# Performance work log

Hardware: AMD Instinct MI355X
Metric: run time of the kernel (lower is better)

Reference implementation:

```python
import jax, jax.numpy as jnp
import numpy as np

USER = 100000
ITEM = 50000
N = USER + ITEM
LATDIM = 64
IMG_DIM = 1024
E_ADJ = 3_000_000
E_IMG = 1_000_000
GNN_LAYERS = 2
RIS_LAMBDA = 1.0
EPS = 1e-12


def spmm(rows, cols, vals, x):
    # sparse [N,N] @ dense [N,D] via gather + segment-sum
    return jax.ops.segment_sum(vals[:, None] * x[cols], rows, num_segments=N)


def setup_inputs() -> dict:
    key = jax.random.key(0)
    ks = jax.random.split(key, 10)
    return {
        "adj_rows": jax.random.randint(ks[0], (E_ADJ,), 0, N, dtype=jnp.int32),
        "adj_cols": jax.random.randint(ks[1], (E_ADJ,), 0, N, dtype=jnp.int32),
        "adj_vals": jax.random.uniform(ks[2], (E_ADJ,), dtype=jnp.float32),
        "img_rows": jax.random.randint(ks[3], (E_IMG,), 0, N, dtype=jnp.int32),
        "img_cols": jax.random.randint(ks[4], (E_IMG,), 0, N, dtype=jnp.int32),
        "img_vals": jax.random.uniform(ks[5], (E_IMG,), dtype=jnp.float32),
        "image_embedding": jax.random.normal(ks[6], (ITEM, IMG_DIM), dtype=jnp.float32),
        "uEmbeds": jax.random.normal(ks[7], (USER, LATDIM), dtype=jnp.float32) * 0.01,
        "iEmbeds": jax.random.normal(ks[8], (ITEM, LATDIM), dtype=jnp.float32) * 0.01,
        "W_trans": jax.random.normal(ks[9], (IMG_DIM, LATDIM), dtype=jnp.float32) * (1.0 / np.sqrt(IMG_DIM)),
        "b_trans": jnp.zeros((LATDIM,), dtype=jnp.float32),
    }


def reference(adj_rows, adj_cols, adj_vals, img_rows, img_cols, img_vals,
              image_embedding, uEmbeds, iEmbeds, W_trans, b_trans):
    # trans == 1: Linear projection of image features
    image_feats = image_embedding @ W_trans + b_trans  # [ITEM, LATDIM]

    # image_adj @ concat(u, i)
    embeds_img_adj = spmm(img_rows, img_cols, img_vals, jnp.concatenate([uEmbeds, iEmbeds], axis=0))

    # F.normalize(image_feats) along dim=1 (L2, eps=1e-12)
    nrm = jnp.linalg.norm(image_feats, axis=1, keepdims=True)
    feats_n = image_feats / jnp.maximum(nrm, EPS)

    embeds_image = spmm(adj_rows, adj_cols, adj_vals, jnp.concatenate([uEmbeds, feats_n], axis=0))
    embeds_image_ = spmm(adj_rows, adj_cols, adj_vals,
                         jnp.concatenate([embeds_image[:USER], iEmbeds], axis=0))
    embeds_image = embeds_image + embeds_image_ + RIS_LAMBDA * embeds_img_adj

    # stacked GCN layers with sum over all layer outputs (including input)
    acc = embeds_image
    cur = embeds_image
    for _ in range(GNN_LAYERS):
        cur = spmm(adj_rows, adj_cols, adj_vals, cur)
        acc = acc + cur

    return acc[:USER], acc[USER:]
```

## Files before the change

### kernel.cpp

```cpp
#include <hip/hip_runtime.h>
#include <hip/hip_fp16.h>

#define USER_N 100000
#define ITEM_N 50000
#define NN (USER_N + ITEM_N)
#define D 64
#define IMGD 1024
#define LDP 68

#define BUCKET_BITS 10
#define BROWS (1 << BUCKET_BITS)
#define NBUCK ((NN + BROWS - 1) >> BUCKET_BITS)
#define CHUNK 4096

typedef _Float16 v4h __attribute__((ext_vector_type(4)));
typedef _Float16 v8h __attribute__((ext_vector_type(8)));
typedef float v4f __attribute__((ext_vector_type(4)));

__global__ __launch_bounds__(256) void wt_prep(
    const float* __restrict__ W, _Float16* __restrict__ Wt16)
{
    const int id = blockIdx.x * 256 + threadIdx.x;
    if (id >= D * IMGD) return;
    const int c = id >> 10;
    const int k = id & 1023;
    Wt16[id] = (_Float16)W[(size_t)k * D + c];
}

#define GAS 72
__global__ __launch_bounds__(256) void gemm_mfma(
    const float* __restrict__ A, const _Float16* __restrict__ Wt16,
    const float* __restrict__ b, float* __restrict__ C)
{
    __shared__ _Float16 Af[64][GAS];
    const int t = threadIdx.x;
    const int w = t >> 6;
    const int lane = t & 63;
    const int l16 = lane & 15;
    const int g = lane >> 4;
    const int row0 = blockIdx.x * 64;

    v4f acc[4] = {};

    const int lr = t >> 4;
    const int lk = (t & 15) * 4;

    for (int k0 = 0; k0 < IMGD; k0 += 64) {
#pragma unroll
        for (int i = 0; i < 4; i++) {
            const int r = lr + i * 16;
            const int grow = row0 + r;
            float4 v = make_float4(0.f, 0.f, 0.f, 0.f);
            if (grow < ITEM_N)
                v = *reinterpret_cast<const float4*>(&A[(size_t)grow * IMGD + k0 + lk]);
            v4h h;
            h[0] = (_Float16)v.x; h[1] = (_Float16)v.y;
            h[2] = (_Float16)v.z; h[3] = (_Float16)v.w;
            *reinterpret_cast<v4h*>(&Af[r][lk]) = h;
        }
        __syncthreads();
#pragma unroll
        for (int s = 0; s < 2; s++) {
            const int kb = s * 32;
            union { v8h v; v4h h[2]; } af;
            af.h[0] = *reinterpret_cast<const v4h*>(&Af[w * 16 + l16][kb + g * 4]);
            af.h[1] = *reinterpret_cast<const v4h*>(&Af[w * 16 + l16][kb + 16 + g * 4]);
#pragma unroll
            for (int n = 0; n < 4; n++) {
                const _Float16* wp = Wt16 + (size_t)(n * 16 + l16) * IMGD + k0 + kb + g * 4;
                union { v8h v; v4h h[2]; } bf;
                bf.h[0] = *reinterpret_cast<const v4h*>(wp);
                bf.h[1] = *reinterpret_cast<const v4h*>(wp + 16);
                acc[n] = __builtin_amdgcn_mfma_f32_16x16x32_f16(af.v, bf.v, acc[n], 0, 0, 0);
            }
        }
        __syncthreads();
    }
#pragma unroll
    for (int n = 0; n < 4; n++) {
        const int col = n * 16 + l16;
        const float bias = b[col];
#pragma unroll
        for (int r = 0; r < 4; r++) {
            const int grow = row0 + w * 16 + g * 4 + r;
            if (grow < ITEM_N)
                C[(size_t)grow * D + col] = acc[n][r] + bias;
        }
    }
}

__global__ __launch_bounds__(256) void gemm_feats32(
    const float* __restrict__ A, const float* __restrict__ W,
    const float* __restrict__ b, float* __restrict__ C)
{
    __shared__ float As[32][LDP];
    __shared__ float Ws[64][LDP];
    const int row0 = blockIdx.x * 32;
    const int t = threadIdx.x;
    const int tx = t & 15, ty = t >> 4;
    float acc[2][4] = {};

    const int lr = t >> 4;
    const int lk = (t & 15) * 4;

    for (int k0 = 0; k0 < IMGD; k0 += 64) {
#pragma unroll
        for (int i = 0; i < 2; i++) {
            const int r = lr + i * 16;
            const int grow = row0 + r;
            float4 v = make_float4(0.f, 0.f, 0.f, 0.f);
            if (grow < ITEM_N)
                v = *reinterpret_cast<const float4*>(&A[(size_t)grow * IMGD + k0 + lk]);
            *reinterpret_cast<float4*>(&As[r][lk]) = v;
        }
#pragma unroll
        for (int i = 0; i < 4; i++) {
            const int kr = lr + i * 16;
            float4 v = *reinterpret_cast<const float4*>(&W[(size_t)(k0 + kr) * D + lk]);
            *reinterpret_cast<float4*>(&Ws[kr][lk]) = v;
        }
        __syncthreads();
#pragma unroll
        for (int kb = 0; kb < 16; kb++) {
            float a_[2][4], w_[4][4];
#pragma unroll
            for (int i = 0; i < 2; i++) {
                const float4 v = *reinterpret_cast<const float4*>(&As[ty * 2 + i][kb * 4]);
                a_[i][0] = v.x; a_[i][1] = v.y; a_[i][2] = v.z; a_[i][3] = v.w;
            }
#pragma unroll
            for (int j = 0; j < 4; j++) {
                const float4 v = *reinterpret_cast<const float4*>(&Ws[kb * 4 + j][tx * 4]);
                w_[j][0] = v.x; w_[j][1] = v.y; w_[j][2] = v.z; w_[j][3] = v.w;
            }
#pragma unroll
            for (int j = 0; j < 4; j++)
#pragma unroll
                for (int i = 0; i < 2; i++)
#pragma unroll
                    for (int c = 0; c < 4; c++)
                        acc[i][c] += a_[i][j] * w_[j][c];
        }
        __syncthreads();
    }
    const float4 bias = *reinterpret_cast<const float4*>(&b[tx * 4]);
#pragma unroll
    for (int i = 0; i < 2; i++) {
        const int grow = row0 + ty * 2 + i;
        if (grow < ITEM_N) {
            float4 v;
            v.x = acc[i][0] + bias.x;
            v.y = acc[i][1] + bias.y;
            v.z = acc[i][2] + bias.z;
            v.w = acc[i][3] + bias.w;
            *reinterpret_cast<float4*>(&C[(size_t)grow * D + tx * 4]) = v;
        }
    }
}

__global__ __launch_bounds__(256) void rownorm_h(
    const float* __restrict__ X, __half* __restrict__ Y, int nrows)
{
    const int gid = blockIdx.x * blockDim.x + threadIdx.x;
    const int row = gid >> 6;
    const int lane = threadIdx.x & 63;
    if (row >= nrows) return;
    float v = X[(size_t)row * D + lane];
    float s = v * v;
#pragma unroll
    for (int o = 32; o > 0; o >>= 1) s += __shfl_xor(s, o, 64);
    const float scale = 1.0f / fmaxf(sqrtf(s), 1e-12f);
    Y[(size_t)row * D + lane] = __float2half(v * scale);
}

__global__ __launch_bounds__(256) void rownorm(float* __restrict__ X, int nrows)
{
    const int gid = blockIdx.x * blockDim.x + threadIdx.x;
    const int row = gid >> 6;
    const int lane = threadIdx.x & 63;
    if (row >= nrows) return;
    float v = X[(size_t)row * D + lane];
    float s = v * v;
#pragma unroll
    for (int o = 32; o > 0; o >>= 1) s += __shfl_xor(s, o, 64);
    const float scale = 1.0f / fmaxf(sqrtf(s), 1e-12f);
    X[(size_t)row * D + lane] = v * scale;
}

__global__ __launch_bounds__(256) void cvt_f2h(
    const float* __restrict__ s, __half* __restrict__ d, int n4)
{
    const int i = blockIdx.x * blockDim.x + threadIdx.x;
    if (i >= n4) return;
    const float4 v = reinterpret_cast<const float4*>(s)[i];
    __half2* d2 = reinterpret_cast<__half2*>(d);
    d2[2 * i]     = __floats2half2_rn(v.x, v.y);
    d2[2 * i + 1] = __floats2half2_rn(v.z, v.w);
}

__global__ __launch_bounds__(256) void bucket_count(
    const int* __restrict__ rows, int nnz, int nb, int* __restrict__ histT)
{
    __shared__ int cnt[NBUCK];
    for (int i = threadIdx.x; i < NBUCK; i += 256) cnt[i] = 0;
    __syncthreads();
    const int e0 = blockIdx.x * CHUNK;
    const int e1 = min(e0 + CHUNK, nnz);
    for (int e = e0 + threadIdx.x; e < e1; e += 256)
        atomicAdd(&cnt[rows[e] >> BUCKET_BITS], 1);
    __syncthreads();
    for (int b = threadIdx.x; b < NBUCK; b += 256)
        histT[b * nb + blockIdx.x] = cnt[b];
}

__global__ __launch_bounds__(1024) void scanA(
    const int* __restrict__ cnt, int* __restrict__ excl,
    int* __restrict__ blocksums, int n)
{
    const int t = threadIdx.x;
    const int gid = blockIdx.x * 1024 + t;
    const int lane = t & 63, wid = t >> 6;
    int v = (gid < n) ? cnt[gid] : 0;
    int x = v;
#pragma unroll
    for (int o = 1; o < 64; o <<= 1) {
        int y = __shfl_up(x, o, 64);
        if (lane >= o) x += y;
    }
    __shared__ int ws[16];
    __shared__ int wo[16];
    if (lane == 63) ws[wid] = x;
    __syncthreads();
    if (t < 16) {
        int s = ws[t];
        int xx = s;
#pragma unroll
        for (int o = 1; o < 16; o <<= 1) {
            int y = __shfl_up(xx, o, 16);
            if (t >= o) xx += y;
        }
        wo[t] = xx - s;
        if (t == 15) blocksums[blockIdx.x] = xx;
    }
    __syncthreads();
    if (gid < n) excl[gid] = x - v + wo[wid];
}

__global__ __launch_bounds__(1024) void scanB(int* __restrict__ bs, int nb)
{
    const int t = threadIdx.x;
    const int lane = t & 63, wid = t >> 6;
    int v = (t < nb) ? bs[t] : 0;
    int x = v;
#pragma unroll
    for (int o = 1; o < 64; o <<= 1) {
        int y = __shfl_up(x, o, 64);
        if (lane >= o) x += y;
    }
    __shared__ int ws[16];
    __shared__ int wo[16];
    if (lane == 63) ws[wid] = x;
    __syncthreads();
    if (t < 16) {
        int s = ws[t];
        int xx = s;
#pragma unroll
        for (int o = 1; o < 16; o <<= 1) {
            int y = __shfl_up(xx, o, 16);
            if (t >= o) xx += y;
        }
        wo[t] = xx - s;
    }
    __syncthreads();
    if (t < nb) bs[t] = x - v + wo[wid];
}

__global__ __launch_bounds__(256) void scan_apply(
    int* __restrict__ excl, const int* __restrict__ bo, int n)
{
    const int gid = blockIdx.x * blockDim.x + threadIdx.x;
    if (gid < n) excl[gid] += bo[gid >> 10];
}

__global__ __launch_bounds__(256) void bucket_place(
    const int* __restrict__ rows, const int* __restrict__ cols,
    const float* __restrict__ vals, int nnz, int nb,
    const int* __restrict__ offsT, uint2* __restrict__ rec)
{
    __shared__ int cur[NBUCK];
    for (int b = threadIdx.x; b < NBUCK; b += 256)
        cur[b] = offsT[b * nb + blockIdx.x];
    __syncthreads();
    const int e0 = blockIdx.x * CHUNK;
    const int e1 = min(e0 + CHUNK, nnz);
    for (int e = e0 + threadIdx.x; e < e1; e += 256) {
        const int r = rows[e];
        const int b = r >> BUCKET_BITS;
        const int pos = atomicAdd(&cur[b], 1);
        rec[pos] = make_uint2(((unsigned)cols[e] << BUCKET_BITS) |
                                  (unsigned)(r & (BROWS - 1)),
                              __float_as_uint(vals[e]));
    }
}

__global__ __launch_bounds__(1024) void bucket_finalize(
    const uint2* __restrict__ rec, int nnz, int nb,
    const int* __restrict__ offsT, int* __restrict__ rp,
    int2* __restrict__ ev)
{
    const int b = blockIdx.x;
    const int t = threadIdx.x;
    const int rlo = b << BUCKET_BITS;
    const int segs = offsT[b * nb];
    const int sege = (b + 1 < NBUCK) ? offsT[(b + 1) * nb] : nnz;

    __shared__ int cnt[BROWS];
    __shared__ int cur[BROWS];
    cnt[t] = 0;
    __syncthreads();
    for (int i = segs + t; i < sege; i += 1024)
        atomicAdd(&cnt[rec[i].x & (BROWS - 1)], 1);
    __syncthreads();

    const int lane = t & 63, wid = t >> 6;
    const int v = cnt[t];
    int x = v;
#pragma unroll
    for (int o = 1; o < 64; o <<= 1) {
        int y = __shfl_up(x, o, 64);
        if (lane >= o) x += y;
    }
    __shared__ int wsum[16];
    __shared__ int woff[16];
    if (lane == 63) wsum[wid] = x;
    __syncthreads();
    if (t < 16) {
        int s = wsum[t];
        int xx = s;
#pragma unroll
        for (int o = 1; o < 16; o <<= 1) {
            int y = __shfl_up(xx, o, 16);
            if (t >= o) xx += y;
        }
        woff[t] = xx - s;
    }
    __syncthreads();
    const int start = segs + (x - v + woff[wid]);

    if (rlo + t < NN) rp[rlo + t] = start;
    if (b == NBUCK - 1 && t == 0) rp[NN] = nnz;
    cur[t] = start;
    __syncthreads();

    for (int i = segs + t; i < sege; i += 1024) {
        const uint2 R = rec[i];
        const int rl = (int)(R.x & (BROWS - 1));
        const int c = (int)(R.x >> BUCKET_BITS);
        const int pos = atomicAdd(&cur[rl], 1);
        ev[pos] = make_int2(c, (int)R.y);
    }
}

__global__ __launch_bounds__(256) void spmm_h4(
    const int* __restrict__ rp, const int2* __restrict__ ev,
    const __half* __restrict__ src,
    float* __restrict__ out32, __half* __restrict__ out16, int limit16,
    const float* __restrict__ add1, const float* __restrict__ add2)
{
    const int wid = (blockIdx.x * 256 + threadIdx.x) >> 6;
    const int lane = threadIdx.x & 63;
    const int sub = lane >> 4;
    const int l16 = lane & 15;
    const int rowbase = wid * 4;
    if (rowbase >= NN) return;
    const int row = rowbase + sub;

    int v = 0;
    if (lane <= 4 && rowbase + lane <= NN) v = rp[rowbase + lane];
    const int s = __shfl(v, sub, 64);
    const int e = __shfl(v, sub + 1, 64);

    const __half* srcl = src + l16 * 4;
    float4 acc = make_float4(0.f, 0.f, 0.f, 0.f);

    union cvt { unsigned u; __half2 h; };
    int i = s;
    for (; i + 3 < e; i += 4) {
        const int2 E0 = ev[i], E1 = ev[i + 1], E2 = ev[i + 2], E3 = ev[i + 3];
        const uint2 g0 = *reinterpret_cast<const uint2*>(srcl + (size_t)E0.x * D);
        const uint2 g1 = *reinterpret_cast<const uint2*>(srcl + (size_t)E1.x * D);
        const uint2 g2 = *reinterpret_cast<const uint2*>(srcl + (size_t)E2.x * D);
        const uint2 g3 = *reinterpret_cast<const uint2*>(srcl + (size_t)E3.x * D);
#pragma unroll
        for (int k = 0; k < 4; k++) {
            const uint2 g = k == 0 ? g0 : k == 1 ? g1 : k == 2 ? g2 : g3;
            const float w = __int_as_float(k == 0 ? E0.y : k == 1 ? E1.y
                                           : k == 2 ? E2.y : E3.y);
            cvt c0, c1; c0.u = g.x; c1.u = g.y;
            const float2 f0 = __half22float2(c0.h);
            const float2 f1 = __half22float2(c1.h);
            acc.x += w * f0.x;
            acc.y += w * f0.y;
            acc.z += w * f1.x;
            acc.w += w * f1.y;
        }
    }
    for (; i < e; i++) {
        const int2 E0 = ev[i];
        const uint2 g = *reinterpret_cast<const uint2*>(srcl + (size_t)E0.x * D);
        const float w = __int_as_float(E0.y);
        cvt c0, c1; c0.u = g.x; c1.u = g.y;
        const float2 f0 = __half22float2(c0.h);
        const float2 f1 = __half22float2(c1.h);
        acc.x += w * f0.x;
        acc.y += w * f0.y;
        acc.z += w * f1.x;
        acc.w += w * f1.y;
    }

    if (row >= NN) return;
    const size_t idx = (size_t)row * D + l16 * 4;
    if (add1) {
        const float4 a = *reinterpret_cast<const float4*>(&add1[idx]);
        acc.x += a.x; acc.y += a.y; acc.z += a.z; acc.w += a.w;
    }
    if (add2) {
        const float4 a = *reinterpret_cast<const float4*>(&add2[idx]);
        acc.x += a.x; acc.y += a.y; acc.z += a.z; acc.w += a.w;
    }
    *reinterpret_cast<float4*>(&out32[idx]) = acc;
    if (row < limit16) {
        const __half2 o0 = __floats2half2_rn(acc.x, acc.y);
        const __half2 o1 = __floats2half2_rn(acc.z, acc.w);
        cvt c0, c1; c0.h = o0; c1.h = o1;
        *reinterpret_cast<uint2*>(&out16[idx]) = make_uint2(c0.u, c1.u);
    }
}

__global__ __launch_bounds__(256) void spmm_csr(
    const int* __restrict__ rp, const int2* __restrict__ ev,
    const float* __restrict__ srcU, const float* __restrict__ srcI,
    float* __restrict__ out,
    const float* __restrict__ add1, const float* __restrict__ add2)
{
    const int gid = blockIdx.x * blockDim.x + threadIdx.x;
    const int row = gid >> 6;
    const int lane = threadIdx.x & 63;
    if (row >= NN) return;
    const int s = rp[row], e = rp[row + 1];
    float acc = 0.f;
    int i = s;
    for (; i + 3 < e; i += 4) {
        const int2 e0 = ev[i], e1 = ev[i + 1], e2 = ev[i + 2], e3 = ev[i + 3];
        const float* p0 = (e0.x < USER_N) ? (srcU + (size_t)e0.x * D)
                                          : (srcI + (size_t)(e0.x - USER_N) * D);
        const float* p1 = (e1.x < USER_N) ? (srcU + (size_t)e1.x * D)
                                          : (srcI + (size_t)(e1.x - USER_N) * D);
        const float* p2 = (e2.x < USER_N) ? (srcU + (size_t)e2.x * D)
                                          : (srcI + (size_t)(e2.x - USER_N) * D);
        const float* p3 = (e3.x < USER_N) ? (srcU + (size_t)e3.x * D)
                                          : (srcI + (size_t)(e3.x - USER_N) * D);
        acc += __int_as_float(e0.y) * p0[lane];
        acc += __int_as_float(e1.y) * p1[lane];
        acc += __int_as_float(e2.y) * p2[lane];
        acc += __int_as_float(e3.y) * p3[lane];
    }
    for (; i < e; i++) {
        const int2 e0 = ev[i];
        const float* p0 = (e0.x < USER_N) ? (srcU + (size_t)e0.x * D)
                                          : (srcI + (size_t)(e0.x - USER_N) * D);
        acc += __int_as_float(e0.y) * p0[lane];
    }
    const size_t idx = (size_t)row * D + lane;
    if (add1) acc += add1[idx];
    if (add2) acc += add2[idx];
    out[idx] = acc;
}

extern "C" void kernel_launch(void* const* d_in, const int* in_sizes, int n_in,
                              void* d_out, int out_size, void* d_ws, size_t ws_size,
                              hipStream_t stream)
{
    const int*   adj_rows = (const int*)d_in[0];
    const int*   adj_cols = (const int*)d_in[1];
    const float* adj_vals = (const float*)d_in[2];
    const int*   img_rows = (const int*)d_in[3];
    const int*   img_cols = (const int*)d_in[4];
    const float* img_vals = (const float*)d_in[5];
    const float* img_emb  = (const float*)d_in[6];
    const float* uEmb     = (const float*)d_in[7];
    const float* iEmb     = (const float*)d_in[8];
    const float* Wt       = (const float*)d_in[9];
    const float* bt       = (const float*)d_in[10];
    float* out = (float*)d_out;

    const int e_adj = in_sizes[0];
    const int e_img = in_sizes[3];
    const int e_max = e_adj > e_img ? e_adj : e_img;
    const int NB_adj = (e_adj + CHUNK - 1) / CHUNK;
    const int NB_img = (e_img + CHUNK - 1) / CHUNK;
    const int NB_max = NB_adj > NB_img ? NB_adj : NB_img;

    const size_t ndbytes = (size_t)NN * D * sizeof(float);
    const size_t nhbytes = (size_t)NN * D * sizeof(__half);

    size_t off = 0;
    auto carve = [&](size_t bytes) { size_t p = off; off += (bytes + 255) & ~(size_t)255; return p; };
    char* base = (char*)d_ws;
    const size_t o_featsN = carve((size_t)ITEM_N * D * sizeof(float));
    const size_t o_bufA   = carve(ndbytes);
    const size_t o_bufB   = carve(ndbytes);
    const size_t o_rpAdj  = carve((NN + 1) * sizeof(int));
    const size_t o_rpImg  = carve((NN + 1) * sizeof(int));
    const size_t o_bsums  = carve(1024 * sizeof(int));
    const size_t o_histT  = carve((size_t)NBUCK * NB_max * sizeof(int));
    const size_t o_rec    = carve((size_t)e_max * sizeof(uint2) > nhbytes
                                      ? (size_t)e_max * sizeof(uint2) : nhbytes);
    const size_t o_evAdj  = carve((size_t)e_adj * sizeof(int2));
    const size_t need_base = off;
    const size_t o_evImg  = carve((size_t)e_img * sizeof(int2) > nhbytes
                                      ? (size_t)e_img * sizeof(int2) : nhbytes);
    const size_t o_x0     = carve(nhbytes);
    const size_t o_wt16   = carve((size_t)D * IMGD * sizeof(_Float16));
    const size_t need_h = off;

    if (ws_size < need_base) return;
    const bool use_h = (ws_size >= need_h);

    float* featsN = (float*)(base + o_featsN);
    float* bufA   = (float*)(base + o_bufA);
    float* bufB   = (float*)(base + o_bufB);
    int* rpAdj    = (int*)(base + o_rpAdj);
    int* rpImg    = (int*)(base + o_rpImg);
    int* bsums    = (int*)(base + o_bsums);
    int* histT    = (int*)(base + o_histT);
    uint2* rec    = (uint2*)(base + o_rec);
    int2* evAdj   = (int2*)(base + o_evAdj);
    int2* evImg   = (int2*)(base + o_evImg);
    __half* xC    = (__half*)(base + o_rec);
    __half* xB    = (__half*)(base + o_evImg);
    __half* x0    = (__half*)(base + o_x0);
    _Float16* wt16 = (_Float16*)(base + o_wt16);

    {
        const int n = NBUCK * NB_adj;
        const int nsb = (n + 1023) / 1024;
        bucket_count<<<NB_adj, 256, 0, stream>>>(adj_rows, e_adj, NB_adj, histT);
        scanA<<<nsb, 1024, 0, stream>>>(histT, histT, bsums, n);
        scanB<<<1, 1024, 0, stream>>>(bsums, nsb);
        scan_apply<<<(n + 255) / 256, 256, 0, stream>>>(histT, bsums, n);
        bucket_place<<<NB_adj, 256, 0, stream>>>(
            adj_rows, adj_cols, adj_vals, e_adj, NB_adj, histT, rec);
        bucket_finalize<<<NBUCK, 1024, 0, stream>>>(
            rec, e_adj, NB_adj, histT, rpAdj, evAdj);
    }
    {
        const int n = NBUCK * NB_img;
        const int nsb = (n + 1023) / 1024;
        bucket_count<<<NB_img, 256, 0, stream>>>(img_rows, e_img, NB_img, histT);
        scanA<<<nsb, 1024, 0, stream>>>(histT, histT, bsums, n);
        scanB<<<1, 1024, 0, stream>>>(bsums, nsb);
        scan_apply<<<(n + 255) / 256, 256, 0, stream>>>(histT, bsums, n);
        bucket_place<<<NB_img, 256, 0, stream>>>(
            img_rows, img_cols, img_vals, e_img, NB_img, histT, rec);
        bucket_finalize<<<NBUCK, 1024, 0, stream>>>(
            rec, e_img, NB_img, histT, rpImg, evImg);
    }

    const int SPMM4_GRID = (NN + 15) / 16;
    const int SPMM_GRID = (NN * 64 + 255) / 256;
    const int RN_GRID = (ITEM_N * 64 + 255) / 256;

    if (use_h) {
        __half* x0I = x0 + (size_t)USER_N * D;
        __half* xBI = xB + (size_t)USER_N * D;

        cvt_f2h<<<(USER_N * D / 4 + 255) / 256, 256, 0, stream>>>(
            uEmb, x0, USER_N * D / 4);
        cvt_f2h<<<(ITEM_N * D / 4 + 255) / 256, 256, 0, stream>>>(
            iEmb, x0I, ITEM_N * D / 4);

        spmm_h4<<<SPMM4_GRID, 256, 0, stream>>>(
            rpImg, evImg, x0, bufA, nullptr, 0, nullptr, nullptr);

        wt_prep<<<(D * IMGD + 255) / 256, 256, 0, stream>>>(Wt, wt16);
        gemm_mfma<<<(ITEM_N + 63) / 64, 256, 0, stream>>>(img_emb, wt16, bt, featsN);
        rownorm_h<<<RN_GRID, 256, 0, stream>>>(featsN, x0I, ITEM_N);

        cvt_f2h<<<(ITEM_N * D / 4 + 255) / 256, 256, 0, stream>>>(
            iEmb, xBI, ITEM_N * D / 4);

        spmm_h4<<<SPMM4_GRID, 256, 0, stream>>>(
            rpAdj, evAdj, x0, bufB, xB, USER_N, nullptr, nullptr);

        spmm_h4<<<SPMM4_GRID, 256, 0, stream>>>(
            rpAdj, evAdj, xB, bufA, xC, NN, bufB, bufA);

        spmm_h4<<<SPMM4_GRID, 256, 0, stream>>>(
            rpAdj, evAdj, xC, bufB, x0, NN, nullptr, nullptr);

        spmm_h4<<<SPMM4_GRID, 256, 0, stream>>>(
            rpAdj, evAdj, x0, out, nullptr, 0, bufA, bufB);
    } else {
        gemm_feats32<<<(ITEM_N + 31) / 32, 256, 0, stream>>>(img_emb, Wt, bt, featsN);
        rownorm<<<RN_GRID, 256, 0, stream>>>(featsN, ITEM_N);

        spmm_csr<<<SPMM_GRID, 256, 0, stream>>>(
            rpImg, evImg, uEmb, iEmb, bufA, nullptr, nullptr);
        spmm_csr<<<SPMM_GRID, 256, 0, stream>>>(
            rpAdj, evAdj, uEmb, featsN, bufB, nullptr, nullptr);
        spmm_csr<<<SPMM_GRID, 256, 0, stream>>>(
            rpAdj, evAdj, bufB, iEmb, bufA, bufB, bufA);
        spmm_csr<<<SPMM_GRID, 256, 0, stream>>>(
            rpAdj, evAdj, bufA, bufA + (size_t)USER_N * D, bufB, nullptr, nullptr);
        spmm_csr<<<SPMM_GRID, 256, 0, stream>>>(
            rpAdj, evAdj, bufB, bufB + (size_t)USER_N * D, out, bufA, bufB);
    }
}
```

Before: 613.4 us.

## Double-buffer MFMA GEMM A tiles and widen SpMM gathers to 8 rows per wave

The image-projection GEMM now uses 32-row blocks, with four waves split as a 2x2 over rows and columns. It double-buffers the fp16 A tile in shared memory so the global load of the next K slice overlaps the current MFMA work. The half-precision SpMM kernel now processes 8 rows per wave, with 8 lanes per row each gathering 16 bytes (8 halves) instead of 8 bytes. This gives wider memory transactions and more rows in flight per wave. The changes aim to reduce GEMM load latency and SpMM gather cost, at the cost of more per-lane accumulator registers and more blocks for the GEMM.

```diff
diff --git a/kernel.cpp b/kernel.cpp
--- a/kernel.cpp
+++ b/kernel.cpp
@@ -27,62 +27,80 @@
     Wt16[id] = (_Float16)W[(size_t)k * D + c];
 }
 
-#define GAS 72
-__global__ __launch_bounds__(256) void gemm_mfma(
+#define GAS2 68
+__global__ __launch_bounds__(256) void gemm_mfma2(
     const float* __restrict__ A, const _Float16* __restrict__ Wt16,
     const float* __restrict__ b, float* __restrict__ C)
 {
-    __shared__ _Float16 Af[64][GAS];
+    __shared__ _Float16 Af[2][32][GAS2];
     const int t = threadIdx.x;
     const int w = t >> 6;
     const int lane = t & 63;
     const int l16 = lane & 15;
     const int g = lane >> 4;
-    const int row0 = blockIdx.x * 64;
-
-    v4f acc[4] = {};
-
-    const int lr = t >> 4;
+    const int row0 = blockIdx.x * 32;
+    const int wr = (w >> 1) * 16;
+    const int wc = (w & 1) * 32;
+
+    v4f acc[2] = {};
+
+    const int lrow0 = t >> 4;
+    const int lrow1 = lrow0 + 16;
     const int lk = (t & 15) * 4;
+    const int ga0 = row0 + lrow0, ga1 = row0 + lrow1;
+
+    {
+        float4 v0 = make_float4(0.f, 0.f, 0.f, 0.f), v1 = v0;
+        if (ga0 < ITEM_N) v0 = *reinterpret_cast<const float4*>(&A[(size_t)ga0 * IMGD + lk]);
+        if (ga1 < ITEM_N) v1 = *reinterpret_cast<const float4*>(&A[(size_t)ga1 * IMGD + lk]);
+        v4h h0, h1;
+        h0[0] = (_Float16)v0.x; h0[1] = (_Float16)v0.y; h0[2] = (_Float16)v0.z; h0[3] = (_Float16)v0.w;
+        h1[0] = (_Float16)v1.x; h1[1] = (_Float16)v1.y; h1[2] = (_Float16)v1.z; h1[3] = (_Float16)v1.w;
+        *reinterpret_cast<v4h*>(&Af[0][lrow0][lk]) = h0;
+        *reinterpret_cast<v4h*>(&Af[0][lrow1][lk]) = h1;
+    }
+    __syncthreads();
 
     for (int k0 = 0; k0 < IMGD; k0 += 64) {
-#pragma unroll
-        for (int i = 0; i < 4; i++) {
-            const int r = lr + i * 16;
-            const int grow = row0 + r;
-            float4 v = make_float4(0.f, 0.f, 0.f, 0.f);
-            if (grow < ITEM_N)
-                v = *reinterpret_cast<const float4*>(&A[(size_t)grow * IMGD + k0 + lk]);
-            v4h h;
-            h[0] = (_Float16)v.x; h[1] = (_Float16)v.y;
-            h[2] = (_Float16)v.z; h[3] = (_Float16)v.w;
-            *reinterpret_cast<v4h*>(&Af[r][lk]) = h;
-        }
-        __syncthreads();
+        const int cur = (k0 >> 6) & 1;
+        const bool has_next = (k0 + 64) < IMGD;
+        float4 n0 = make_float4(0.f, 0.f, 0.f, 0.f), n1 = n0;
+        if (has_next) {
+            if (ga0 < ITEM_N) n0 = *reinterpret_cast<const float4*>(&A[(size_t)ga0 * IMGD + k0 + 64 + lk]);
+            if (ga1 < ITEM_N) n1 = *reinterpret_cast<const float4*>(&A[(size_t)ga1 * IMGD + k0 + 64 + lk]);
+        }
 #pragma unroll
         for (int s = 0; s < 2; s++) {
             const int kb = s * 32;
             union { v8h v; v4h h[2]; } af;
-            af.h[0] = *reinterpret_cast<const v4h*>(&Af[w * 16 + l16][kb + g * 4]);
-            af.h[1] = *reinterpret_cast<const v4h*>(&Af[w * 16 + l16][kb + 16 + g * 4]);
-#pragma unroll
-            for (int n = 0; n < 4; n++) {
-                const _Float16* wp = Wt16 + (size_t)(n * 16 + l16) * IMGD + k0 + kb + g * 4;
+            af.h[0] = *reinterpret_cast<const v4h*>(&Af[cur][wr + l16][kb + g * 4]);
+            af.h[1] = *reinterpret_cast<const v4h*>(&Af[cur][wr + l16][kb + 16 + g * 4]);
+#pragma unroll
+            for (int n = 0; n < 2; n++) {
+                const _Float16* wp = Wt16 + (size_t)(wc + n * 16 + l16) * IMGD + k0 + kb + g * 4;
                 union { v8h v; v4h h[2]; } bf;
                 bf.h[0] = *reinterpret_cast<const v4h*>(wp);
                 bf.h[1] = *reinterpret_cast<const v4h*>(wp + 16);
                 acc[n] = __builtin_amdgcn_mfma_f32_16x16x32_f16(af.v, bf.v, acc[n], 0, 0, 0);
             }
         }
-        __syncthreads();
-    }
-#pragma unroll
-    for (int n = 0; n < 4; n++) {
-        const int col = n * 16 + l16;
+        if (has_next) {
+            __syncthreads();
+            v4h h0, h1;
+            h0[0] = (_Float16)n0.x; h0[1] = (_Float16)n0.y; h0[2] = (_Float16)n0.z; h0[3] = (_Float16)n0.w;
+            h1[0] = (_Float16)n1.x; h1[1] = (_Float16)n1.y; h1[2] = (_Float16)n1.z; h1[3] = (_Float16)n1.w;
+            *reinterpret_cast<v4h*>(&Af[cur ^ 1][lrow0][lk]) = h0;
+            *reinterpret_cast<v4h*>(&Af[cur ^ 1][lrow1][lk]) = h1;
+            __syncthreads();
+        }
+    }
+#pragma unroll
+    for (int n = 0; n < 2; n++) {
+        const int col = wc + n * 16 + l16;
         const float bias = b[col];
 #pragma unroll
         for (int r = 0; r < 4; r++) {
-            const int grow = row0 + w * 16 + g * 4 + r;
+            const int grow = row0 + wr + g * 4 + r;
             if (grow < ITEM_N)
                 C[(size_t)grow * D + col] = acc[n][r] + bias;
         }
@@ -361,7 +379,7 @@
     }
 }
 
-__global__ __launch_bounds__(256) void spmm_h4(
+__global__ __launch_bounds__(256) void spmm_h8(
     const int* __restrict__ rp, const int2* __restrict__ ev,
     const __half* __restrict__ src,
     float* __restrict__ out32, __half* __restrict__ out16, int limit16,
@@ -369,71 +387,80 @@
 {
     const int wid = (blockIdx.x * 256 + threadIdx.x) >> 6;
     const int lane = threadIdx.x & 63;
-    const int sub = lane >> 4;
-    const int l16 = lane & 15;
-    const int rowbase = wid * 4;
+    const int sub = lane >> 3;
+    const int l8 = lane & 7;
+    const int rowbase = wid * 8;
     if (rowbase >= NN) return;
     const int row = rowbase + sub;
 
     int v = 0;
-    if (lane <= 4 && rowbase + lane <= NN) v = rp[rowbase + lane];
+    if (lane <= 8 && rowbase + lane <= NN) v = rp[rowbase + lane];
     const int s = __shfl(v, sub, 64);
     const int e = __shfl(v, sub + 1, 64);
 
-    const __half* srcl = src + l16 * 4;
-    float4 acc = make_float4(0.f, 0.f, 0.f, 0.f);
-
-    union cvt { unsigned u; __half2 h; };
+    const __half* srcl = src + l8 * 8;
+    float acc[8] = {};
+
+    union cvt4 { uint4 u; __half2 h[4]; };
     int i = s;
     for (; i + 3 < e; i += 4) {
         const int2 E0 = ev[i], E1 = ev[i + 1], E2 = ev[i + 2], E3 = ev[i + 3];
-        const uint2 g0 = *reinterpret_cast<const uint2*>(srcl + (size_t)E0.x * D);
-        const uint2 g1 = *reinterpret_cast<const uint2*>(srcl + (size_t)E1.x * D);
-        const uint2 g2 = *reinterpret_cast<const uint2*>(srcl + (size_t)E2.x * D);
-        const uint2 g3 = *reinterpret_cast<const uint2*>(srcl + (size_t)E3.x * D);
+        cvt4 g0, g1, g2, g3;
+        g0.u = *reinterpret_cast<const uint4*>(srcl + (size_t)E0.x * D);
+        g1.u = *reinterpret_cast<const uint4*>(srcl + (size_t)E1.x * D);
+        g2.u = *reinterpret_cast<const uint4*>(srcl + (size_t)E2.x * D);
+        g3.u = *reinterpret_cast<const uint4*>(srcl + (size_t)E3.x * D);
 #pragma unroll
         for (int k = 0; k < 4; k++) {
-            const uint2 g = k == 0 ? g0 : k == 1 ? g1 : k == 2 ? g2 : g3;
+            const cvt4& g = k == 0 ? g0 : k == 1 ? g1 : k == 2 ? g2 : g3;
             const float w = __int_as_float(k == 0 ? E0.y : k == 1 ? E1.y
                                            : k == 2 ? E2.y : E3.y);
-            cvt c0, c1; c0.u = g.x; c1.u = g.y;
-            const float2 f0 = __half22float2(c0.h);
-            const float2 f1 = __half22float2(c1.h);
-            acc.x += w * f0.x;
-            acc.y += w * f0.y;
-            acc.z += w * f1.x;
-            acc.w += w * f1.y;
+#pragma unroll
+            for (int j = 0; j < 4; j++) {
+                const float2 f = __half22float2(g.h[j]);
+                acc[2 * j]     += w * f.x;
+                acc[2 * j + 1] += w * f.y;
+            }
         }
     }
     for (; i < e; i++) {
         const int2 E0 = ev[i];
-        const uint2 g = *reinterpret_cast<const uint2*>(srcl + (size_t)E0.x * D);
+        cvt4 g;
+        g.u = *reinterpret_cast<const uint4*>(srcl + (size_t)E0.x * D);
         const float w = __int_as_float(E0.y);
-        cvt c0, c1; c0.u = g.x; c1.u = g.y;
-        const float2 f0 = __half22float2(c0.h);
-        const float2 f1 = __half22float2(c1.h);
-        acc.x += w * f0.x;
-        acc.y += w * f0.y;
-        acc.z += w * f1.x;
-        acc.w += w * f1.y;
+#pragma unroll
+        for (int j = 0; j < 4; j++) {
+            const float2 f = __half22float2(g.h[j]);
+            acc[2 * j]     += w * f.x;
+            acc[2 * j + 1] += w * f.y;
+        }
     }
 
     if (row >= NN) return;
-    const size_t idx = (size_t)row * D + l16 * 4;
-    if (add1) {
-        const float4 a = *reinterpret_cast<const float4*>(&add1[idx]);
-        acc.x += a.x; acc.y += a.y; acc.z += a.z; acc.w += a.w;
-    }
-    if (add2) {
-        const float4 a = *reinterpret_cast<const float4*>(&add2[idx]);
-        acc.x += a.x; acc.y += a.y; acc.z += a.z; acc.w += a.w;
-    }
-    *reinterpret_cast<float4*>(&out32[idx]) = acc;
+    const size_t idx = (size_t)row * D + l8 * 8;
+#pragma unroll
+    for (int h = 0; h < 2; h++) {
+        if (add1) {
+            const float4 a = *reinterpret_cast<const float4*>(&add1[idx + h * 4]);
+            acc[4 * h] += a.x; acc[4 * h + 1] += a.y;
+            acc[4 * h + 2] += a.z; acc[4 * h + 3] += a.w;
+        }
+        if (add2) {
+            const float4 a = *reinterpret_cast<const float4*>(&add2[idx + h * 4]);
+            acc[4 * h] += a.x; acc[4 * h + 1] += a.y;
+            acc[4 * h + 2] += a.z; acc[4 * h + 3] += a.w;
+        }
+        float4 o;
+        o.x = acc[4 * h]; o.y = acc[4 * h + 1];
+        o.z = acc[4 * h + 2]; o.w = acc[4 * h + 3];
+        *reinterpret_cast<float4*>(&out32[idx + h * 4]) = o;
+    }
     if (row < limit16) {
-        const __half2 o0 = __floats2half2_rn(acc.x, acc.y);
-        const __half2 o1 = __floats2half2_rn(acc.z, acc.w);
-        cvt c0, c1; c0.h = o0; c1.h = o1;
-        *reinterpret_cast<uint2*>(&out16[idx]) = make_uint2(c0.u, c1.u);
+        cvt4 o16;
+#pragma unroll
+        for (int j = 0; j < 4; j++)
+            o16.h[j] = __floats2half2_rn(acc[2 * j], acc[2 * j + 1]);
+        *reinterpret_cast<uint4*>(&out16[idx]) = o16.u;
     }
 }
 
@@ -567,7 +594,7 @@
             rec, e_img, NB_img, histT, rpImg, evImg);
     }
 
-    const int SPMM4_GRID = (NN + 15) / 16;
+    const int SPMM8_GRID = (NN + 31) / 32;
     const int SPMM_GRID = (NN * 64 + 255) / 256;
     const int RN_GRID = (ITEM_N * 64 + 255) / 256;
 
@@ -580,26 +607,26 @@
         cvt_f2h<<<(ITEM_N * D / 4 + 255) / 256, 256, 0, stream>>>(
             iEmb, x0I, ITEM_N * D / 4);
 
-        spmm_h4<<<SPMM4_GRID, 256, 0, stream>>>(
+        spmm_h8<<<SPMM8_GRID, 256, 0, stream>>>(
             rpImg, evImg, x0, bufA, nullptr, 0, nullptr, nullptr);
 
         wt_prep<<<(D * IMGD + 255) / 256, 256, 0, stream>>>(Wt, wt16);
-        gemm_mfma<<<(ITEM_N + 63) / 64, 256, 0, stream>>>(img_emb, wt16, bt, featsN);
+        gemm_mfma2<<<(ITEM_N + 31) / 32, 256, 0, stream>>>(img_emb, wt16, bt, featsN);
         rownorm_h<<<RN_GRID, 256, 0, stream>>>(featsN, x0I, ITEM_N);
 
         cvt_f2h<<<(ITEM_N * D / 4 + 255) / 256, 256, 0, stream>>>(
             iEmb, xBI, ITEM_N * D / 4);
 
-        spmm_h4<<<SPMM4_GRID, 256, 0, stream>>>(
+        spmm_h8<<<SPMM8_GRID, 256, 0, stream>>>(
             rpAdj, evAdj, x0, bufB, xB, USER_N, nullptr, nullptr);
 
-        spmm_h4<<<SPMM4_GRID, 256, 0, stream>>>(
+        spmm_h8<<<SPMM8_GRID, 256, 0, stream>>>(
             rpAdj, evAdj, xB, bufA, xC, NN, bufB, bufA);
 
-        spmm_h4<<<SPMM4_GRID, 256, 0, stream>>>(
+        spmm_h8<<<SPMM8_GRID, 256, 0, stream>>>(
             rpAdj, evAdj, xC, bufB, x0, NN, nullptr, nullptr);
 
-        spmm_h4<<<SPMM4_GRID, 256, 0, stream>>>(
+        spmm_h8<<<SPMM8_GRID, 256, 0, stream>>>(
             rpAdj, evAdj, x0, out, nullptr, 0, bufA, bufB);
     } else {
         gemm_feats32<<<(ITEM_N + 31) / 32, 256, 0, stream>>>(img_emb, Wt, bt, featsN);
```

Measured after the change: 598.7 us. 2.4% less time.
